# Kernel optimization log

Hardware: AMD Instinct MI355X
Metric: run time of the kernel (lower is better)

Reference implementation:

```python
import jax, jax.numpy as jnp
import numpy as np

D_MODEL = 1024
N_HEADS = 16
D_HEAD = D_MODEL // N_HEADS
BATCH = 4
SEQ = 2048
NEG_INF = -1e9  # finite large-negative; avoids NaNs on fully-masked rows under jit


def setup_inputs() -> dict:
    key = jax.random.key(0)
    ks = jax.random.split(key, 10)
    xav = np.sqrt(6.0 / (D_MODEL + D_MODEL))  # xavier_uniform bound
    def w(k):
        return jax.random.uniform(k, (D_MODEL, D_MODEL), jnp.float32, -xav, xav)
    return {
        "x": jax.random.normal(ks[0], (BATCH, SEQ, D_MODEL), jnp.float32),
        "attention_mask": jnp.tril(jnp.ones((SEQ, SEQ), jnp.int32)),  # causal: 0 => masked
        "key_padding_mask": jnp.zeros((BATCH, SEQ), jnp.bool_),  # True => masked
        "Wq": w(ks[1]), "bq": jnp.zeros((D_MODEL,), jnp.float32),
        "Wk": w(ks[2]), "bk": jnp.zeros((D_MODEL,), jnp.float32),
        "Wv": w(ks[3]), "bv": jnp.zeros((D_MODEL,), jnp.float32),
        "Wo": w(ks[4]), "bo": jnp.zeros((D_MODEL,), jnp.float32),
    }


def reference(x, attention_mask, key_padding_mask, Wq, bq, Wk, bk, Wv, bv, Wo, bo):
    b, s, d = x.shape
    scale = 1.0 / np.sqrt(D_HEAD)
    # torch Linear: x @ W.T + b
    def proj(W, bias):
        y = jnp.einsum('bsd,ed->bse', x, W) + bias
        return y.reshape(b, s, N_HEADS, D_HEAD).transpose(0, 2, 1, 3)  # (b,h,s,dh)
    q = proj(Wq, bq)
    k = proj(Wk, bk)
    v = proj(Wv, bv)
    scores = jnp.einsum('bhqd,bhkd->bhqk', q, k) * scale  # (b,h,s,s)
    scores = jnp.where(attention_mask[None, None] == 0, NEG_INF, scores)
    scores = jnp.where(key_padding_mask[:, None, None, :], NEG_INF, scores)
    attn = jax.nn.softmax(scores, axis=-1)
    out = jnp.einsum('bhqk,bhkd->bhqd', attn, v)  # (b,h,s,dh)
    out = out.transpose(0, 2, 1, 3).reshape(b, s, d)
    out = jnp.einsum('bsd,ed->bse', out, Wo) + bo
    return out
```

## Files before the change

kernel.cpp:

```cpp
#include <hip/hip_runtime.h>
#include <stdint.h>

typedef __bf16 bf16;
typedef __bf16 bf16x4 __attribute__((ext_vector_type(4)));
typedef __bf16 bf16x8 __attribute__((ext_vector_type(8)));
typedef float f32x4 __attribute__((ext_vector_type(4)));

typedef __attribute__((address_space(3))) uint32_t lds_u32_t;
typedef const __attribute__((address_space(1))) uint32_t glb_u32_t;

#define MFMA16(a, b, c) __builtin_amdgcn_mfma_f32_16x16x32_bf16((a), (b), (c), 0, 0, 0)

#if __has_builtin(__builtin_amdgcn_exp2f)
#define EXP2(x) __builtin_amdgcn_exp2f(x)
#else
#define EXP2(x) exp2f(x)
#endif

#define SEQ 2048
#define DMODEL 1024
#define NH 16
#define DH 64
#define MTOT 8192

#define BM 128
#define BN 128
#define BK 64
#define NKSTEP (DMODEL / BK)

#define KVB 64

__global__ __launch_bounds__(256) void cvt_f32_bf16(const float* __restrict__ in,
                                                    bf16* __restrict__ out, int n) {
  int i = blockIdx.x * blockDim.x + threadIdx.x;
  int idx = i * 4;
  if (idx < n) {
    float4 v = *reinterpret_cast<const float4*>(in + idx);
    bf16x4 o;
    o[0] = (bf16)v.x; o[1] = (bf16)v.y; o[2] = (bf16)v.z; o[3] = (bf16)v.w;
    *reinterpret_cast<bf16x4*>(out + idx) = o;
  }
}

__global__ __launch_bounds__(256) void cvt_w4(const float* __restrict__ W0,
                                              const float* __restrict__ W1,
                                              const float* __restrict__ W2,
                                              const float* __restrict__ W3,
                                              bf16* __restrict__ o0, bf16* __restrict__ o1,
                                              bf16* __restrict__ o2, bf16* __restrict__ o3) {
  const float* in;
  bf16* out;
  switch (blockIdx.y) {
    case 0: in = W0; out = o0; break;
    case 1: in = W1; out = o1; break;
    case 2: in = W2; out = o2; break;
    default: in = W3; out = o3; break;
  }
  int idx = (blockIdx.x * 256 + threadIdx.x) * 4;
  float4 v = *reinterpret_cast<const float4*>(in + idx);
  bf16x4 o;
  o[0] = (bf16)v.x; o[1] = (bf16)v.y; o[2] = (bf16)v.z; o[3] = (bf16)v.w;
  *reinterpret_cast<bf16x4*>(out + idx) = o;
}

static __device__ __forceinline__ void stage16(const bf16* g, const bf16* l) {
  __builtin_amdgcn_global_load_lds((glb_u32_t*)g, (lds_u32_t*)l, 16, 0, 0);
}

static __device__ __forceinline__ void stage_tile(const bf16* __restrict__ src, int row0,
                                                  int col0, bf16* ldsbase, int w, int lane) {
#pragma unroll
  for (int i = 0; i < 4; ++i) {
    int ci = w * 4 + i;
    int r = ci * 8 + (lane >> 3);
    int c = (((lane & 7) ^ (r & 7)) << 3);
    stage16(src + (size_t)(row0 + r) * 1024 + col0 + c, ldsbase + ci * 512);
  }
}

static __device__ __forceinline__ bf16x8 frag_ld(const bf16* base, int row, int col) {
  uint32_t byte = ((uint32_t)(row * BK + col) * 2u) ^ (uint32_t)((row & 7) << 4);
  return *reinterpret_cast<const bf16x8*>(reinterpret_cast<const char*>(base) + byte);
}

static __device__ __forceinline__ void gemm_core(const bf16* __restrict__ A,
                                                 const bf16* __restrict__ B, int m0, int n0,
                                                 int w, int lane, bf16* As, bf16* Bs,
                                                 f32x4 acc[4][4]) {
  const int wm = w >> 1, wn = w & 1;
  const int cA = lane & 15, gA = lane >> 4;

  stage_tile(A, m0, 0, As, w, lane);
  stage_tile(B, n0, 0, Bs, w, lane);
  __syncthreads();

  for (int t = 0; t < NKSTEP; ++t) {
    const int buf = t & 1;
    bf16* Acur = As + buf * (BM * BK);
    bf16* Bcur = Bs + buf * (BN * BK);
    if (t + 1 < NKSTEP) {
      stage_tile(A, m0, (t + 1) * BK, As + (buf ^ 1) * (BM * BK), w, lane);
      stage_tile(B, n0, (t + 1) * BK, Bs + (buf ^ 1) * (BN * BK), w, lane);
    }
#pragma unroll
    for (int ks = 0; ks < 2; ++ks) {
      bf16x8 af[4], bfr[4];
#pragma unroll
      for (int i = 0; i < 4; ++i)
        af[i] = frag_ld(Acur, wm * 64 + i * 16 + cA, ks * 32 + gA * 8);
#pragma unroll
      for (int i = 0; i < 4; ++i)
        bfr[i] = frag_ld(Bcur, wn * 64 + i * 16 + cA, ks * 32 + gA * 8);
#pragma unroll
      for (int mi = 0; mi < 4; ++mi)
#pragma unroll
        for (int ni = 0; ni < 4; ++ni)
          acc[mi][ni] = MFMA16(af[mi], bfr[ni], acc[mi][ni]);
    }
    __syncthreads();
  }
}

__global__ __launch_bounds__(256) void qkv_gemm(
    const bf16* __restrict__ X, const bf16* __restrict__ Wq, const bf16* __restrict__ Wk,
    const bf16* __restrict__ Wv, const float* __restrict__ bq, const float* __restrict__ bk,
    const float* __restrict__ bv, bf16* __restrict__ Qo, bf16* __restrict__ Ko,
    bf16* __restrict__ Vt) {
  __shared__ bf16 As[2 * BM * BK];
  __shared__ bf16 Bs[2 * BN * BK];
  const int tid = threadIdx.x;
  const int w = tid >> 6, lane = tid & 63;
  const int mt = blockIdx.x, nt = blockIdx.y;
  const int ysel = nt >> 3;
  const int n0 = (nt & 7) * BN;
  const int m0 = mt * BM;
  const bf16* W = (ysel == 0) ? Wq : ((ysel == 1) ? Wk : Wv);
  const float* bias = (ysel == 0) ? bq : ((ysel == 1) ? bk : bv);

  f32x4 acc[4][4];
  const f32x4 fz = {0.f, 0.f, 0.f, 0.f};
#pragma unroll
  for (int i = 0; i < 4; ++i)
#pragma unroll
    for (int j = 0; j < 4; ++j) acc[i][j] = fz;

  gemm_core(X, W, m0, n0, w, lane, As, Bs, acc);

  const int wm = w >> 1, wn = w & 1;
  const int cA = lane & 15, gA = lane >> 4;

  if (ysel == 2) {
#pragma unroll
    for (int mi = 0; mi < 4; ++mi)
#pragma unroll
      for (int ni = 0; ni < 4; ++ni) {
        int e = n0 + wn * 64 + ni * 16 + cA;
        int h = e >> 6, dh = e & 63;
        int m = m0 + wm * 64 + mi * 16 + gA * 4;
        int b = m >> 11, s = m & 2047;
        float bb = bias[e];
        f32x4 v = acc[mi][ni];
        bf16x4 o;
        o[0] = (bf16)(v[0] + bb); o[1] = (bf16)(v[1] + bb);
        o[2] = (bf16)(v[2] + bb); o[3] = (bf16)(v[3] + bb);
        *reinterpret_cast<bf16x4*>(Vt + ((size_t)((b * NH + h) * DH + dh)) * SEQ + s) = o;
      }
  } else {
    bf16* dst = (ysel == 0) ? Qo : Ko;
    const float qs = (ysel == 0) ? 0.125f * 1.44269504f : 1.0f;
#pragma unroll
    for (int mi = 0; mi < 4; ++mi)
#pragma unroll
      for (int ni = 0; ni < 4; ++ni) {
        int e = n0 + wn * 64 + ni * 16 + cA;
        int h = e >> 6, dh = e & 63;
        int m = m0 + wm * 64 + mi * 16 + gA * 4;
        int b = m >> 11, s = m & 2047;
        float bb = bias[e];
        f32x4 v = acc[mi][ni];
        size_t base = ((size_t)(b * NH + h) * SEQ + s) * DH + dh;
#pragma unroll
        for (int j = 0; j < 4; ++j) dst[base + (size_t)j * DH] = (bf16)((v[j] + bb) * qs);
      }
  }
}

__global__ __launch_bounds__(256) void out_gemm(const bf16* __restrict__ A,
                                                const bf16* __restrict__ Wo,
                                                const float* __restrict__ bo,
                                                float* __restrict__ Out) {
  __shared__ bf16 As[2 * BM * BK];
  __shared__ bf16 Bs[2 * BN * BK];
  const int tid = threadIdx.x;
  const int w = tid >> 6, lane = tid & 63;
  const int m0 = blockIdx.x * BM;
  const int n0 = blockIdx.y * BN;

  f32x4 acc[4][4];
  const f32x4 fz = {0.f, 0.f, 0.f, 0.f};
#pragma unroll
  for (int i = 0; i < 4; ++i)
#pragma unroll
    for (int j = 0; j < 4; ++j) acc[i][j] = fz;

  gemm_core(A, Wo, m0, n0, w, lane, As, Bs, acc);

  const int wm = w >> 1, wn = w & 1;
  const int cA = lane & 15, gA = lane >> 4;
#pragma unroll
  for (int mi = 0; mi < 4; ++mi)
#pragma unroll
    for (int ni = 0; ni < 4; ++ni) {
      int e = n0 + wn * 64 + ni * 16 + cA;
      int m = m0 + wm * 64 + mi * 16 + gA * 4;
      float bb = bo[e];
      f32x4 v = acc[mi][ni];
#pragma unroll
      for (int j = 0; j < 4; ++j) Out[(size_t)(m + j) * DMODEL + e] = v[j] + bb;
    }
}

__global__ __launch_bounds__(256) void flash_attn(const bf16* __restrict__ Q,
                                                  const bf16* __restrict__ K,
                                                  const bf16* __restrict__ Vt,
                                                  bf16* __restrict__ O) {
  __shared__ bf16 Ks[2][KVB * DH];
  __shared__ bf16 Vs[2][DH * KVB];
  __shared__ bf16 Plds[4 * 32 * 72];
  const int tid = threadIdx.x;
  const int w = tid >> 6, lane = tid & 63;
  const int bh = blockIdx.x;
  const int y = blockIdx.y;
  const int cA = lane & 15, gA = lane >> 4;
  const int l8 = lane & 7, r8 = lane >> 3;
  const int sb = lane & 48;

  const bf16* Qp = Q + (size_t)bh * SEQ * DH;
  const bf16* Kp = K + (size_t)bh * SEQ * DH;
  const bf16* Vp = Vt + (size_t)bh * DH * SEQ;
  const int b = bh >> 4, h = bh & 15;

  const uint32_t swz = (uint32_t)(cA & 7) << 4;
  const uint32_t lo0 = (uint32_t)cA * 128 + (((uint32_t)gA * 16) ^ swz);
  const uint32_t lo1 = (uint32_t)cA * 128 + ((64u + (uint32_t)gA * 16) ^ swz);
  char* pbase = (char*)Plds + w * 4608;

#define STAGE_K(dst, kv)                                                          \
  {                                                                               \
    _Pragma("unroll") for (int i = 0; i < 2; ++i) {                               \
      int ci = w * 2 + i;                                                         \
      int r = ci * 8 + r8;                                                        \
      int c = ((l8 ^ (r & 7)) << 3);                                              \
      stage16(Kp + (size_t)((kv) + r) * DH + c, (dst) + ci * 512);                \
    }                                                                             \
  }
#define STAGE_V(dst, kv)                                                          \
  {                                                                               \
    _Pragma("unroll") for (int i = 0; i < 2; ++i) {                               \
      int ci = w * 2 + i;                                                         \
      int r = ci * 8 + r8;                                                        \
      int c = ((l8 ^ (r & 7)) << 3);                                              \
      stage16(Vp + (size_t)r * SEQ + (kv) + c, (dst) + ci * 512);                 \
    }                                                                             \
  }

  const f32x4 fz = {0.f, 0.f, 0.f, 0.f};

  for (int phase = 0; phase < 2; ++phase) {
    const int qt = phase ? y : (15 - y);
    const int nt = (qt + 1) * 2;
    const int q0w = qt * 128 + w * 32;
    const int qmax = q0w + 31;

    bf16x8 qf[2][2];
#pragma unroll
    for (int qp = 0; qp < 2; ++qp)
#pragma unroll
      for (int ks = 0; ks < 2; ++ks)
        qf[qp][ks] = *reinterpret_cast<const bf16x8*>(
            Qp + (size_t)(q0w + qp * 16 + cA) * DH + ks * 32 + gA * 8);

    f32x4 o_acc[2][4];
#pragma unroll
    for (int qp = 0; qp < 2; ++qp)
#pragma unroll
      for (int dt = 0; dt < 4; ++dt) o_acc[qp][dt] = fz;
    float m_s[2] = {-1e30f, -1e30f}, l_s[2] = {0.f, 0.f};

    int cur = 0;
    STAGE_K(Ks[0], 0)
    STAGE_V(Vs[0], 0)
    __syncthreads();

    for (int it = 0; it < nt; ++it) {
      const int kv = it * KVB;
      if (it + 1 < nt) {
        STAGE_K(Ks[cur ^ 1], kv + KVB)
        STAGE_V(Vs[cur ^ 1], kv + KVB)
      }
      if (kv <= qmax) {
        const char* kc = (const char*)&Ks[cur][0];
        const char* vc = (const char*)&Vs[cur][0];

        bf16x8 kfr[4][2];
#pragma unroll
        for (int kt = 0; kt < 4; ++kt) {
          kfr[kt][0] = *reinterpret_cast<const bf16x8*>(kc + lo0 + kt * 2048);
          kfr[kt][1] = *reinterpret_cast<const bf16x8*>(kc + lo1 + kt * 2048);
        }

        f32x4 s[4][2];
        __builtin_amdgcn_s_setprio(1);
#pragma unroll
        for (int kt = 0; kt < 4; ++kt)
#pragma unroll
          for (int qp = 0; qp < 2; ++qp) {
            s[kt][qp] = MFMA16(kfr[kt][0], qf[qp][0], fz);
            s[kt][qp] = MFMA16(kfr[kt][1], qf[qp][1], s[kt][qp]);
          }
        __builtin_amdgcn_s_setprio(0);

#pragma unroll
        for (int qp = 0; qp < 2; ++qp) {
          if (kv + 63 > q0w + qp * 16) {
            const int q = q0w + qp * 16 + cA;
#pragma unroll
            for (int kt = 0; kt < 4; ++kt) {
              const int kb = kv + kt * 16 + gA * 4;
#pragma unroll
              for (int j = 0; j < 4; ++j)
                if (kb + j > q) s[kt][qp][j] = -1e30f;
            }
          }
        }

#pragma unroll
        for (int qp = 0; qp < 2; ++qp) {
          float r =
              fmaxf(fmaxf(fmaxf(s[0][qp][0], s[0][qp][1]), fmaxf(s[0][qp][2], s[0][qp][3])),
                    fmaxf(fmaxf(s[1][qp][0], s[1][qp][1]), fmaxf(s[1][qp][2], s[1][qp][3])));
          float r2 =
              fmaxf(fmaxf(fmaxf(s[2][qp][0], s[2][qp][1]), fmaxf(s[2][qp][2], s[2][qp][3])),
                    fmaxf(fmaxf(s[3][qp][0], s[3][qp][1]), fmaxf(s[3][qp][2], s[3][qp][3])));
          r = fmaxf(r, r2);
          r = fmaxf(r, __shfl_xor(r, 16));
          r = fmaxf(r, __shfl_xor(r, 32));

          const float mo = m_s[qp];
          float mn = mo;
          if (!__all(r <= mo + 12.0f)) {
            mn = fmaxf(mo, r);
            m_s[qp] = mn;
            const float scl = EXP2(mo - mn);
            float sclr[4];
#pragma unroll
            for (int j = 0; j < 4; ++j) sclr[j] = __shfl(scl, sb | (4 * gA + j));
#pragma unroll
            for (int dt = 0; dt < 4; ++dt) {
              f32x4 t = o_acc[qp][dt];
              t[0] *= sclr[0]; t[1] *= sclr[1]; t[2] *= sclr[2]; t[3] *= sclr[3];
              o_acc[qp][dt] = t;
            }
            l_s[qp] *= scl;
          }

          float rs = 0.f;
#pragma unroll
          for (int kt = 0; kt < 4; ++kt) {
            float p0 = EXP2(s[kt][qp][0] - mn);
            float p1 = EXP2(s[kt][qp][1] - mn);
            float p2 = EXP2(s[kt][qp][2] - mn);
            float p3 = EXP2(s[kt][qp][3] - mn);
            s[kt][qp][0] = p0; s[kt][qp][1] = p1; s[kt][qp][2] = p2; s[kt][qp][3] = p3;
            rs += (p0 + p1) + (p2 + p3);
          }
          rs += __shfl_xor(rs, 16);
          rs += __shfl_xor(rs, 32);
          l_s[qp] += rs;

#pragma unroll
          for (int kt = 0; kt < 4; ++kt) {
            bf16x4 t;
            t[0] = (bf16)s[kt][qp][0]; t[1] = (bf16)s[kt][qp][1];
            t[2] = (bf16)s[kt][qp][2]; t[3] = (bf16)s[kt][qp][3];
            *reinterpret_cast<bf16x4*>(pbase + (qp * 16 + cA) * 144 + kt * 32 + gA * 8) = t;
          }
        }

        bf16x8 pf[2][2];
#pragma unroll
        for (int qp = 0; qp < 2; ++qp) {
          pf[qp][0] = *reinterpret_cast<const bf16x8*>(pbase + (qp * 16 + cA) * 144 + gA * 16);
          pf[qp][1] =
              *reinterpret_cast<const bf16x8*>(pbase + (qp * 16 + cA) * 144 + 64 + gA * 16);
        }

        __builtin_amdgcn_s_setprio(1);
#pragma unroll
        for (int dt = 0; dt < 4; ++dt) {
          bf16x8 vf0 = *reinterpret_cast<const bf16x8*>(vc + lo0 + dt * 2048);
          bf16x8 vf1 = *reinterpret_cast<const bf16x8*>(vc + lo1 + dt * 2048);
#pragma unroll
          for (int qp = 0; qp < 2; ++qp) {
            o_acc[qp][dt] = MFMA16(pf[qp][0], vf0, o_acc[qp][dt]);
            o_acc[qp][dt] = MFMA16(pf[qp][1], vf1, o_acc[qp][dt]);
          }
        }
        __builtin_amdgcn_s_setprio(0);
      }
      __syncthreads();
      cur ^= 1;
    }

#pragma unroll
    for (int qp = 0; qp < 2; ++qp) {
      const float li = 1.0f / l_s[qp];
      float lrow[4];
#pragma unroll
      for (int j = 0; j < 4; ++j) lrow[j] = __shfl(li, sb | (4 * gA + j));
#pragma unroll
      for (int dt = 0; dt < 4; ++dt) {
        const int dh = dt * 16 + cA;
#pragma unroll
        for (int j = 0; j < 4; ++j) {
          const int srow = q0w + qp * 16 + gA * 4 + j;
          O[((size_t)(b * SEQ + srow)) * DMODEL + h * DH + dh] =
              (bf16)(o_acc[qp][dt][j] * lrow[j]);
        }
      }
    }
    __syncthreads();
  }
}

extern "C" void kernel_launch(void* const* d_in, const int* in_sizes, int n_in, void* d_out,
                              int out_size, void* d_ws, size_t ws_size, hipStream_t stream) {
  const float* x = (const float*)d_in[0];
  const float* Wq = (const float*)d_in[3];
  const float* bq = (const float*)d_in[4];
  const float* Wk = (const float*)d_in[5];
  const float* bk = (const float*)d_in[6];
  const float* Wv = (const float*)d_in[7];
  const float* bv = (const float*)d_in[8];
  const float* Wo = (const float*)d_in[9];
  const float* bo = (const float*)d_in[10];
  float* out = (float*)d_out;

  char* ws = (char*)d_ws;
  bf16* xb = (bf16*)(ws + 0);
  bf16* wqb = (bf16*)(ws + 16777216);
  bf16* wkb = (bf16*)(ws + 18874368);
  bf16* wvb = (bf16*)(ws + 20971520);
  bf16* wob = (bf16*)(ws + 23068672);
  bf16* Qb = (bf16*)(ws + 25165824);
  bf16* Kb = (bf16*)(ws + 41943040);
  bf16* Vt = (bf16*)(ws + 58720256);
  bf16* Ab = xb;

  cvt_f32_bf16<<<8192, 256, 0, stream>>>(x, xb, MTOT * DMODEL);
  cvt_w4<<<dim3(1024, 4), 256, 0, stream>>>(Wq, Wk, Wv, Wo, wqb, wkb, wvb, wob);

  qkv_gemm<<<dim3(64, 24), 256, 0, stream>>>(xb, wqb, wkb, wvb, bq, bk, bv, Qb, Kb, Vt);
  flash_attn<<<dim3(64, 8), 256, 0, stream>>>(Qb, Kb, Vt, Ab);
  out_gemm<<<dim3(64, 8), 256, 0, stream>>>(Ab, wob, bo, out);
}
```

Measured before the change: 196.6 us.

## Rewrite projection GEMMs as 256x128 tiles with 8 waves and triple-buffered pipeline

Replaces the 128x128 double-buffered GEMM core with a 256x128 tile computed by 512 threads. A is staged through a triple-buffered LDS ring and B is double-buffered, with explicit vmcnt/lgkmcnt waits, raw barriers and setprio around the MFMA bursts so loads overlap compute. The goal is to cut LDS and global traffic per FLOP and hide load latency better. In exchange it uses more LDS per block and leaves fewer blocks to spread across CUs. The hand-placed waits and the clamped prefetch indices are fragile, and the epilogue's wm/wn mapping may not match the eight-wave layout.

```diff
diff --git a/kernel.cpp b/kernel.cpp
--- a/kernel.cpp
+++ b/kernel.cpp
@@ -23,12 +23,20 @@
 #define DH 64
 #define MTOT 8192
 
-#define BM 128
-#define BN 128
-#define BK 64
-#define NKSTEP (DMODEL / BK)
-
 #define KVB 64
+
+#define VMW(n) asm volatile("s_waitcnt vmcnt(" #n ")" ::: "memory")
+#define LGKM0()                                         \
+  {                                                     \
+    asm volatile("s_waitcnt lgkmcnt(0)" ::: "memory");  \
+    __builtin_amdgcn_sched_barrier(0);                  \
+  }
+#define BARR()                                          \
+  {                                                     \
+    asm volatile("" ::: "memory");                      \
+    __builtin_amdgcn_s_barrier();                       \
+    asm volatile("" ::: "memory");                      \
+  }
 
 __global__ __launch_bounds__(256) void cvt_f32_bf16(const float* __restrict__ in,
                                                     bf16* __restrict__ out, int n) {
@@ -67,73 +75,123 @@
   __builtin_amdgcn_global_load_lds((glb_u32_t*)g, (lds_u32_t*)l, 16, 0, 0);
 }
 
-static __device__ __forceinline__ void stage_tile(const bf16* __restrict__ src, int row0,
-                                                  int col0, bf16* ldsbase, int w, int lane) {
-#pragma unroll
-  for (int i = 0; i < 4; ++i) {
-    int ci = w * 4 + i;
-    int r = ci * 8 + (lane >> 3);
-    int c = (((lane & 7) ^ (r & 7)) << 3);
-    stage16(src + (size_t)(row0 + r) * 1024 + col0 + c, ldsbase + ci * 512);
-  }
-}
-
 static __device__ __forceinline__ bf16x8 frag_ld(const bf16* base, int row, int col) {
-  uint32_t byte = ((uint32_t)(row * BK + col) * 2u) ^ (uint32_t)((row & 7) << 4);
+  uint32_t byte = ((uint32_t)(row * 64 + col) * 2u) ^ (uint32_t)((row & 7) << 4);
   return *reinterpret_cast<const bf16x8*>(reinterpret_cast<const char*>(base) + byte);
 }
 
-static __device__ __forceinline__ void gemm_core(const bf16* __restrict__ A,
-                                                 const bf16* __restrict__ B, int m0, int n0,
-                                                 int w, int lane, bf16* As, bf16* Bs,
-                                                 f32x4 acc[4][4]) {
+static __device__ __forceinline__ void gemm256(const bf16* __restrict__ A,
+                                               const bf16* __restrict__ B, int m0, int n0,
+                                               int w, int lane, bf16* As, bf16* Bs,
+                                               f32x4 acc[4][4]) {
   const int wm = w >> 1, wn = w & 1;
   const int cA = lane & 15, gA = lane >> 4;
-
-  stage_tile(A, m0, 0, As, w, lane);
-  stage_tile(B, n0, 0, Bs, w, lane);
-  __syncthreads();
-
-  for (int t = 0; t < NKSTEP; ++t) {
-    const int buf = t & 1;
-    bf16* Acur = As + buf * (BM * BK);
-    bf16* Bcur = Bs + buf * (BN * BK);
-    if (t + 1 < NKSTEP) {
-      stage_tile(A, m0, (t + 1) * BK, As + (buf ^ 1) * (BM * BK), w, lane);
-      stage_tile(B, n0, (t + 1) * BK, Bs + (buf ^ 1) * (BN * BK), w, lane);
-    }
-#pragma unroll
-    for (int ks = 0; ks < 2; ++ks) {
-      bf16x8 af[4], bfr[4];
-#pragma unroll
-      for (int i = 0; i < 4; ++i)
-        af[i] = frag_ld(Acur, wm * 64 + i * 16 + cA, ks * 32 + gA * 8);
-#pragma unroll
-      for (int i = 0; i < 4; ++i)
-        bfr[i] = frag_ld(Bcur, wn * 64 + i * 16 + cA, ks * 32 + gA * 8);
-#pragma unroll
-      for (int mi = 0; mi < 4; ++mi)
-#pragma unroll
-        for (int ni = 0; ni < 4; ++ni)
-          acc[mi][ni] = MFMA16(af[mi], bfr[ni], acc[mi][ni]);
-    }
-    __syncthreads();
-  }
-}
-
-__global__ __launch_bounds__(256) void qkv_gemm(
+  const int r8 = lane >> 3;
+  const int csw = ((lane & 7) ^ r8) << 3;
+
+#define SA_(half, kk, buf)                                                         \
+  {                                                                                \
+    _Pragma("unroll") for (int i_ = 0; i_ < 2; ++i_) {                             \
+      int ci_ = w * 2 + i_;                                                        \
+      stage16(A + (size_t)(m0 + (half)*128 + ci_ * 8 + r8) * 1024 + (kk) + csw,    \
+              As + (buf)*16384 + (half)*8192 + ci_ * 512);                         \
+    }                                                                              \
+  }
+#define SB_(kk, buf)                                                               \
+  {                                                                                \
+    _Pragma("unroll") for (int i_ = 0; i_ < 2; ++i_) {                             \
+      int ci_ = w * 2 + i_;                                                        \
+      stage16(B + (size_t)(n0 + ci_ * 8 + r8) * 1024 + (kk) + csw,                 \
+              Bs + (buf)*8192 + ci_ * 512);                                        \
+    }                                                                              \
+  }
+#define CL3(x) ((x) < 16 ? (x) : (x)-3)
+#define CL2(x) ((x) < 16 ? (x) : (x)-2)
+
+  SA_(0, 0, 0)
+  SA_(1, 0, 0)
+  SB_(0, 0)
+  SA_(0, 64, 1)
+  VMW(2);
+  BARR();
+
+  int cur = 0, nxt = 1, nx2 = 2;
+  bf16x8 aA[2][2], bB[4][2];
+
+  for (int t = 0; t < 16; ++t) {
+    const int bcur = t & 1;
+    const bf16* Ac = As + cur * 16384;
+    const bf16* Bc = Bs + bcur * 8192;
+
+#pragma unroll
+    for (int mi2 = 0; mi2 < 2; ++mi2)
+#pragma unroll
+      for (int ks = 0; ks < 2; ++ks)
+        aA[mi2][ks] = frag_ld(Ac, wm * 64 + mi2 * 16 + cA, ks * 32 + gA * 8);
+#pragma unroll
+    for (int ni = 0; ni < 4; ++ni)
+#pragma unroll
+      for (int ks = 0; ks < 2; ++ks)
+        bB[ni][ks] = frag_ld(Bc, wn * 64 + ni * 16 + cA, ks * 32 + gA * 8);
+
+    SA_(1, CL3(t + 1) * 64, nxt)
+    SB_(CL2(t + 1) * 64, bcur ^ 1)
+
+    BARR();
+    LGKM0();
+    __builtin_amdgcn_s_setprio(1);
+#pragma unroll
+    for (int mi2 = 0; mi2 < 2; ++mi2)
+#pragma unroll
+      for (int ni = 0; ni < 4; ++ni) {
+        acc[mi2][ni] = MFMA16(aA[mi2][0], bB[ni][0], acc[mi2][ni]);
+        acc[mi2][ni] = MFMA16(aA[mi2][1], bB[ni][1], acc[mi2][ni]);
+      }
+    __builtin_amdgcn_s_setprio(0);
+    BARR();
+
+#pragma unroll
+    for (int mi2 = 0; mi2 < 2; ++mi2)
+#pragma unroll
+      for (int ks = 0; ks < 2; ++ks)
+        aA[mi2][ks] = frag_ld(Ac, wm * 64 + 32 + mi2 * 16 + cA, ks * 32 + gA * 8);
+
+    SA_(0, CL3(t + 2) * 64, nx2)
+
+    VMW(2);
+    BARR();
+    LGKM0();
+    __builtin_amdgcn_s_setprio(1);
+#pragma unroll
+    for (int mi2 = 0; mi2 < 2; ++mi2)
+#pragma unroll
+      for (int ni = 0; ni < 4; ++ni) {
+        acc[2 + mi2][ni] = MFMA16(aA[mi2][0], bB[ni][0], acc[2 + mi2][ni]);
+        acc[2 + mi2][ni] = MFMA16(aA[mi2][1], bB[ni][1], acc[2 + mi2][ni]);
+      }
+    __builtin_amdgcn_s_setprio(0);
+    BARR();
+
+    const int r_ = cur; cur = nxt; nxt = nx2; nx2 = r_;
+  }
+#undef SA_
+#undef SB_
+#undef CL3
+#undef CL2
+}
+
+__global__ __launch_bounds__(512, 2) void qkv_gemm(
     const bf16* __restrict__ X, const bf16* __restrict__ Wq, const bf16* __restrict__ Wk,
     const bf16* __restrict__ Wv, const float* __restrict__ bq, const float* __restrict__ bk,
     const float* __restrict__ bv, bf16* __restrict__ Qo, bf16* __restrict__ Ko,
     bf16* __restrict__ Vt) {
-  __shared__ bf16 As[2 * BM * BK];
-  __shared__ bf16 Bs[2 * BN * BK];
+  __shared__ bf16 As[3 * 16384];
+  __shared__ bf16 Bs[2 * 8192];
   const int tid = threadIdx.x;
   const int w = tid >> 6, lane = tid & 63;
-  const int mt = blockIdx.x, nt = blockIdx.y;
-  const int ysel = nt >> 3;
-  const int n0 = (nt & 7) * BN;
-  const int m0 = mt * BM;
+  const int ysel = blockIdx.y >> 3;
+  const int n0 = (blockIdx.y & 7) * 128;
+  const int m0 = blockIdx.x * 256;
   const bf16* W = (ysel == 0) ? Wq : ((ysel == 1) ? Wk : Wv);
   const float* bias = (ysel == 0) ? bq : ((ysel == 1) ? bk : bv);
 
@@ -144,7 +202,7 @@
 #pragma unroll
     for (int j = 0; j < 4; ++j) acc[i][j] = fz;
 
-  gemm_core(X, W, m0, n0, w, lane, As, Bs, acc);
+  gemm256(X, W, m0, n0, w, lane, As, Bs, acc);
 
   const int wm = w >> 1, wn = w & 1;
   const int cA = lane & 15, gA = lane >> 4;
@@ -185,16 +243,16 @@
   }
 }
 
-__global__ __launch_bounds__(256) void out_gemm(const bf16* __restrict__ A,
-                                                const bf16* __restrict__ Wo,
-                                                const float* __restrict__ bo,
-                                                float* __restrict__ Out) {
-  __shared__ bf16 As[2 * BM * BK];
-  __shared__ bf16 Bs[2 * BN * BK];
+__global__ __launch_bounds__(512, 2) void out_gemm(const bf16* __restrict__ A,
+                                                   const bf16* __restrict__ Wo,
+                                                   const float* __restrict__ bo,
+                                                   float* __restrict__ Out) {
+  __shared__ bf16 As[3 * 16384];
+  __shared__ bf16 Bs[2 * 8192];
   const int tid = threadIdx.x;
   const int w = tid >> 6, lane = tid & 63;
-  const int m0 = blockIdx.x * BM;
-  const int n0 = blockIdx.y * BN;
+  const int m0 = blockIdx.x * 256;
+  const int n0 = blockIdx.y * 128;
 
   f32x4 acc[4][4];
   const f32x4 fz = {0.f, 0.f, 0.f, 0.f};
@@ -203,7 +261,7 @@
 #pragma unroll
     for (int j = 0; j < 4; ++j) acc[i][j] = fz;
 
-  gemm_core(A, Wo, m0, n0, w, lane, As, Bs, acc);
+  gemm256(A, Wo, m0, n0, w, lane, As, Bs, acc);
 
   const int wm = w >> 1, wn = w & 1;
   const int cA = lane & 15, gA = lane >> 4;
@@ -460,7 +518,7 @@
   cvt_f32_bf16<<<8192, 256, 0, stream>>>(x, xb, MTOT * DMODEL);
   cvt_w4<<<dim3(1024, 4), 256, 0, stream>>>(Wq, Wk, Wv, Wo, wqb, wkb, wvb, wob);
 
-  qkv_gemm<<<dim3(64, 24), 256, 0, stream>>>(xb, wqb, wkb, wvb, bq, bk, bv, Qb, Kb, Vt);
+  qkv_gemm<<<dim3(32, 24), 512, 0, stream>>>(xb, wqb, wkb, wvb, bq, bk, bv, Qb, Kb, Vt);
   flash_attn<<<dim3(64, 8), 256, 0, stream>>>(Qb, Kb, Vt, Ab);
-  out_gemm<<<dim3(64, 8), 256, 0, stream>>>(Ab, wob, bo, out);
-}
+  out_gemm<<<dim3(32, 8), 512, 0, stream>>>(Ab, wob, bo, out);
+}
```

New measurement: 182.4 us. 7.2% less time.
